# Performance work log

Measured on AMD Instinct MI355X. Metric: run time of the kernel, lower is better.

The kernel has to match this reference:

```python
import jax, jax.numpy as jnp
import numpy as np

DT = 0.001  # forward-arg default in the original module
EPS = 1e-10


def setup_inputs() -> dict:
    key = jax.random.key(0)
    k1, k2 = jax.random.split(key)
    x = jax.random.normal(k1, (5000, 512, 16), dtype=jnp.float32)  # [nt, traces, channels]
    y = jax.random.normal(k2, (5000, 512, 16), dtype=jnp.float32)
    return {"x": x, "y": y}


def reference(x, y):
    # Per-(t,c) L2 norms over time axis (dim 0): shape [T, C]
    xnorm = jnp.linalg.norm(x, ord=2, axis=0) + EPS
    ynorm = jnp.linalg.norm(y, ord=2, axis=0) + EPS
    # Per-(t,c) dot products over time: shape [T, C]
    dots = jnp.einsum('ntc,ntc->tc', x, y)
    # cc = -dot(xn * dt, yn) = -dt * dot(x, y) / (||x|| * ||y||)
    cc = -DT * dots / (xnorm * ynorm)
    # Original skips slices where max|x| == 0 (contributes 0.0)
    mask = jnp.max(jnp.abs(x), axis=0) > 0
    return jnp.sum(jnp.where(mask, cc, jnp.zeros_like(cc)))
```

## Files before the change

kernel.cpp:

```cpp
#include <hip/hip_runtime.h>
#include <hip/hip_bf16.h>
#include <math.h>


#define NT_TOTAL 5000
#define NCOL     8192
#define NCOL4    2048

__global__ __launch_bounds__(256) void ncc_partial(const float4* __restrict__ x,
                                                   const float4* __restrict__ y,
                                                   float4* __restrict__ ws,
                                                   int clen, int nchunk) {
    const int col4 = blockIdx.x * 256 + threadIdx.x;
    const int ch   = blockIdx.y;
    int n0 = ch * clen;
    int n1 = n0 + clen;
    if (n1 > NT_TOTAL) n1 = NT_TOTAL;
    const int steps = (n1 > n0) ? (n1 - n0) : 0;

    const float4* xp = x + (size_t)n0 * NCOL4 + col4;
    const float4* yp = y + (size_t)n0 * NCOL4 + col4;

    float4 sxx = make_float4(0.f, 0.f, 0.f, 0.f);
    float4 syy = make_float4(0.f, 0.f, 0.f, 0.f);
    float4 sxy = make_float4(0.f, 0.f, 0.f, 0.f);
    float4 mx  = make_float4(0.f, 0.f, 0.f, 0.f);

#define ACC(a, b)                                                     \
    sxx.x = fmaf(a.x, a.x, sxx.x); sxx.y = fmaf(a.y, a.y, sxx.y);     \
    sxx.z = fmaf(a.z, a.z, sxx.z); sxx.w = fmaf(a.w, a.w, sxx.w);     \
    syy.x = fmaf(b.x, b.x, syy.x); syy.y = fmaf(b.y, b.y, syy.y);     \
    syy.z = fmaf(b.z, b.z, syy.z); syy.w = fmaf(b.w, b.w, syy.w);     \
    sxy.x = fmaf(a.x, b.x, sxy.x); sxy.y = fmaf(a.y, b.y, sxy.y);     \
    sxy.z = fmaf(a.z, b.z, sxy.z); sxy.w = fmaf(a.w, b.w, sxy.w);     \
    mx.x = fmaxf(mx.x, fabsf(a.x)); mx.y = fmaxf(mx.y, fabsf(a.y));   \
    mx.z = fmaxf(mx.z, fabsf(a.z)); mx.w = fmaxf(mx.w, fabsf(a.w))

    int i = 0;
    for (; i + 8 <= steps; i += 8) {
        float4 a0 = xp[0 * NCOL4];
        float4 a1 = xp[1 * NCOL4];
        float4 a2 = xp[2 * NCOL4];
        float4 a3 = xp[3 * NCOL4];
        float4 a4 = xp[4 * NCOL4];
        float4 a5 = xp[5 * NCOL4];
        float4 a6 = xp[6 * NCOL4];
        float4 a7 = xp[7 * NCOL4];
        float4 b0 = yp[0 * NCOL4];
        float4 b1 = yp[1 * NCOL4];
        float4 b2 = yp[2 * NCOL4];
        float4 b3 = yp[3 * NCOL4];
        float4 b4 = yp[4 * NCOL4];
        float4 b5 = yp[5 * NCOL4];
        float4 b6 = yp[6 * NCOL4];
        float4 b7 = yp[7 * NCOL4];
        xp += 8 * NCOL4;
        yp += 8 * NCOL4;
        ACC(a0, b0); ACC(a1, b1); ACC(a2, b2); ACC(a3, b3);
        ACC(a4, b4); ACC(a5, b5); ACC(a6, b6); ACC(a7, b7);
    }
    for (; i < steps; ++i) {
        float4 a = xp[0];
        float4 b = yp[0];
        xp += NCOL4;
        yp += NCOL4;
        ACC(a, b);
    }
#undef ACC

    float4* SXX = ws;
    float4* SYY = ws + (size_t)nchunk * NCOL4;
    float4* SXY = ws + (size_t)2 * nchunk * NCOL4;
    float4* MX  = ws + (size_t)3 * nchunk * NCOL4;
    const size_t idx = (size_t)ch * NCOL4 + col4;
    SXX[idx] = sxx;
    SYY[idx] = syy;
    SXY[idx] = sxy;
    MX[idx]  = mx;
}

__global__ __launch_bounds__(256) void ncc_combine(const float4* __restrict__ ws4,
                                                   float* __restrict__ partials,
                                                   int nchunk) {
    const int lane  = threadIdx.x & 63;
    const int strip = threadIdx.x >> 6;
    const int c4    = blockIdx.x * 64 + lane;
    const int NC4   = NCOL4;

    const float4* SXX = ws4;
    const float4* SYY = ws4 + (size_t)nchunk * NC4;
    const float4* SXY = ws4 + (size_t)2 * nchunk * NC4;
    const float4* MX  = ws4 + (size_t)3 * nchunk * NC4;

    const int spc = (nchunk + 3) / 4;
    int ch0 = strip * spc;
    int ch1 = ch0 + spc;
    if (ch1 > nchunk) ch1 = nchunk;

    float4 sxx = make_float4(0.f, 0.f, 0.f, 0.f);
    float4 syy = make_float4(0.f, 0.f, 0.f, 0.f);
    float4 sxy = make_float4(0.f, 0.f, 0.f, 0.f);
    float4 mx  = make_float4(0.f, 0.f, 0.f, 0.f);
    for (int ch = ch0; ch < ch1; ++ch) {
        const size_t idx = (size_t)ch * NC4 + c4;
        float4 a = SXX[idx], b = SYY[idx], d = SXY[idx], m = MX[idx];
        sxx.x += a.x; sxx.y += a.y; sxx.z += a.z; sxx.w += a.w;
        syy.x += b.x; syy.y += b.y; syy.z += b.z; syy.w += b.w;
        sxy.x += d.x; sxy.y += d.y; sxy.z += d.z; sxy.w += d.w;
        mx.x = fmaxf(mx.x, m.x); mx.y = fmaxf(mx.y, m.y);
        mx.z = fmaxf(mx.z, m.z); mx.w = fmaxf(mx.w, m.w);
    }

    __shared__ float4 LXX[4][64], LYY[4][64], LXY[4][64], LMX[4][64];
    LXX[strip][lane] = sxx;
    LYY[strip][lane] = syy;
    LXY[strip][lane] = sxy;
    LMX[strip][lane] = mx;
    __syncthreads();

    if (strip == 0) {
        for (int s = 1; s < 4; ++s) {
            float4 a = LXX[s][lane], b = LYY[s][lane], d = LXY[s][lane], m = LMX[s][lane];
            sxx.x += a.x; sxx.y += a.y; sxx.z += a.z; sxx.w += a.w;
            syy.x += b.x; syy.y += b.y; syy.z += b.z; syy.w += b.w;
            sxy.x += d.x; sxy.y += d.y; sxy.z += d.z; sxy.w += d.w;
            mx.x = fmaxf(mx.x, m.x); mx.y = fmaxf(mx.y, m.y);
            mx.z = fmaxf(mx.z, m.z); mx.w = fmaxf(mx.w, m.w);
        }
        float cc = 0.f;
        if (mx.x > 0.f) cc += -0.001f * sxy.x / ((sqrtf(sxx.x) + 1e-10f) * (sqrtf(syy.x) + 1e-10f));
        if (mx.y > 0.f) cc += -0.001f * sxy.y / ((sqrtf(sxx.y) + 1e-10f) * (sqrtf(syy.y) + 1e-10f));
        if (mx.z > 0.f) cc += -0.001f * sxy.z / ((sqrtf(sxx.z) + 1e-10f) * (sqrtf(syy.z) + 1e-10f));
        if (mx.w > 0.f) cc += -0.001f * sxy.w / ((sqrtf(sxx.w) + 1e-10f) * (sqrtf(syy.w) + 1e-10f));

        for (int off = 32; off > 0; off >>= 1)
            cc += __shfl_down(cc, off);
        if (lane == 0)
            partials[blockIdx.x] = cc;
    }
}

__global__ __launch_bounds__(64) void ncc_final(const float* __restrict__ partials,
                                                float* __restrict__ out) {
    float v = (threadIdx.x < 32) ? partials[threadIdx.x] : 0.f;
    for (int off = 32; off > 0; off >>= 1)
        v += __shfl_down(v, off);
    if (threadIdx.x == 0) out[0] = v;
}

extern "C" void kernel_launch(void* const* d_in, const int* in_sizes, int n_in,
                              void* d_out, int out_size, void* d_ws, size_t ws_size,
                              hipStream_t stream) {
    const float* x = (const float*)d_in[0];
    const float* y = (const float*)d_in[1];
    float* out = (float*)d_out;
    float* ws  = (float*)d_ws;

    const size_t per_chunk_bytes = 4ull * NCOL * sizeof(float);
    size_t avail = (ws_size > 256) ? (ws_size - 256) : 0;
    int nchunk = (int)(avail / per_chunk_bytes);
    if (nchunk > 100) nchunk = 100;
    if (nchunk < 1)   nchunk = 1;
    const int clen = (NT_TOTAL + nchunk - 1) / nchunk;

    float* partials = ws + 4ull * (size_t)nchunk * NCOL;

    dim3 g1(NCOL4 / 256, nchunk);
    ncc_partial<<<g1, 256, 0, stream>>>((const float4*)x, (const float4*)y,
                                        (float4*)ws, clen, nchunk);
    ncc_combine<<<32, 256, 0, stream>>>((const float4*)ws, partials, nchunk);
    ncc_final<<<1, 64, 0, stream>>>(partials, out);
}
```

Baseline: 78.22 us.

## Stream inputs via async global-to-LDS loads with double buffering

Replaces direct float4 register loads in the partial-reduction kernel with global_load_lds transfers into double-buffered shared memory. Explicit vmcnt waits overlap the next tile's loads with accumulation of the current one. It also caps the time-chunk count at 64 instead of 100, which reduces the grid size. The cost is more complex synchronisation and fewer resident blocks, which could lower the memory parallelism that hides latency.

```diff
diff --git a/kernel.cpp b/kernel.cpp
--- a/kernel.cpp
+++ b/kernel.cpp
@@ -3,76 +3,108 @@
 #include <math.h>
 
 
-#define NT_TOTAL 5000
+#define NT       5000
+#define NROW_F   8192
 #define NCOL     8192
 #define NCOL4    2048
 
-__global__ __launch_bounds__(256) void ncc_partial(const float4* __restrict__ x,
-                                                   const float4* __restrict__ y,
+typedef __attribute__((address_space(3))) void lds_void;
+typedef const __attribute__((address_space(1))) void gm_void;
+
+__global__ __launch_bounds__(256) void ncc_partial(const float* __restrict__ xg,
+                                                   const float* __restrict__ yg,
                                                    float4* __restrict__ ws,
-                                                   int clen, int nchunk) {
-    const int col4 = blockIdx.x * 256 + threadIdx.x;
+                                                   int clen, int nchunk, int T) {
+    __shared__ float4 BA[4][4][2][64];
+    __shared__ float4 BB[4][4][2][64];
+
+    const int tid  = threadIdx.x;
+    const int w    = tid >> 6;
+    const int lane = tid & 63;
+    const int bx   = blockIdx.x;
     const int ch   = blockIdx.y;
-    int n0 = ch * clen;
-    int n1 = n0 + clen;
-    if (n1 > NT_TOTAL) n1 = NT_TOTAL;
-    const int steps = (n1 > n0) ? (n1 - n0) : 0;
-
-    const float4* xp = x + (size_t)n0 * NCOL4 + col4;
-    const float4* yp = y + (size_t)n0 * NCOL4 + col4;
+    const int n0   = ch * clen;
+    int n1 = n0 + clen; if (n1 > NT) n1 = NT;
+
+    const int colf = bx * 1024 + tid * 4;
 
     float4 sxx = make_float4(0.f, 0.f, 0.f, 0.f);
     float4 syy = make_float4(0.f, 0.f, 0.f, 0.f);
     float4 sxy = make_float4(0.f, 0.f, 0.f, 0.f);
     float4 mx  = make_float4(0.f, 0.f, 0.f, 0.f);
 
-#define ACC(a, b)                                                     \
-    sxx.x = fmaf(a.x, a.x, sxx.x); sxx.y = fmaf(a.y, a.y, sxx.y);     \
-    sxx.z = fmaf(a.z, a.z, sxx.z); sxx.w = fmaf(a.w, a.w, sxx.w);     \
-    syy.x = fmaf(b.x, b.x, syy.x); syy.y = fmaf(b.y, b.y, syy.y);     \
-    syy.z = fmaf(b.z, b.z, syy.z); syy.w = fmaf(b.w, b.w, syy.w);     \
-    sxy.x = fmaf(a.x, b.x, sxy.x); sxy.y = fmaf(a.y, b.y, sxy.y);     \
-    sxy.z = fmaf(a.z, b.z, sxy.z); sxy.w = fmaf(a.w, b.w, sxy.w);     \
-    mx.x = fmaxf(mx.x, fabsf(a.x)); mx.y = fmaxf(mx.y, fabsf(a.y));   \
+#define ACC4(a, b)                                                      \
+    sxx.x = fmaf(a.x, a.x, sxx.x); sxx.y = fmaf(a.y, a.y, sxx.y);       \
+    sxx.z = fmaf(a.z, a.z, sxx.z); sxx.w = fmaf(a.w, a.w, sxx.w);       \
+    syy.x = fmaf(b.x, b.x, syy.x); syy.y = fmaf(b.y, b.y, syy.y);       \
+    syy.z = fmaf(b.z, b.z, syy.z); syy.w = fmaf(b.w, b.w, syy.w);       \
+    sxy.x = fmaf(a.x, b.x, sxy.x); sxy.y = fmaf(a.y, b.y, sxy.y);       \
+    sxy.z = fmaf(a.z, b.z, sxy.z); sxy.w = fmaf(a.w, b.w, sxy.w);       \
+    mx.x = fmaxf(mx.x, fabsf(a.x)); mx.y = fmaxf(mx.y, fabsf(a.y));     \
     mx.z = fmaxf(mx.z, fabsf(a.z)); mx.w = fmaxf(mx.w, fabsf(a.w))
 
-    int i = 0;
-    for (; i + 8 <= steps; i += 8) {
-        float4 a0 = xp[0 * NCOL4];
-        float4 a1 = xp[1 * NCOL4];
-        float4 a2 = xp[2 * NCOL4];
-        float4 a3 = xp[3 * NCOL4];
-        float4 a4 = xp[4 * NCOL4];
-        float4 a5 = xp[5 * NCOL4];
-        float4 a6 = xp[6 * NCOL4];
-        float4 a7 = xp[7 * NCOL4];
-        float4 b0 = yp[0 * NCOL4];
-        float4 b1 = yp[1 * NCOL4];
-        float4 b2 = yp[2 * NCOL4];
-        float4 b3 = yp[3 * NCOL4];
-        float4 b4 = yp[4 * NCOL4];
-        float4 b5 = yp[5 * NCOL4];
-        float4 b6 = yp[6 * NCOL4];
-        float4 b7 = yp[7 * NCOL4];
-        xp += 8 * NCOL4;
-        yp += 8 * NCOL4;
-        ACC(a0, b0); ACC(a1, b1); ACC(a2, b2); ACC(a3, b3);
-        ACC(a4, b4); ACC(a5, b5); ACC(a6, b6); ACC(a7, b7);
-    }
-    for (; i < steps; ++i) {
-        float4 a = xp[0];
-        float4 b = yp[0];
-        xp += NCOL4;
-        yp += NCOL4;
-        ACC(a, b);
-    }
-#undef ACC
+#define ISSUE(BUF, t)                                                         \
+    {                                                                         \
+        _Pragma("unroll")                                                     \
+        for (int r = 0; r < 4; ++r) {                                         \
+            int n = n0 + (t) * 4 + r;                                         \
+            if (n > NT - 1) n = NT - 1;                                       \
+            const float* px = xg + (size_t)n * NROW_F + colf;                 \
+            const float* py = yg + (size_t)n * NROW_F + colf;                 \
+            __builtin_amdgcn_global_load_lds((gm_void*)px,                    \
+                (lds_void*)&BUF[w][r][0][0], 16, 0, 0);                       \
+            __builtin_amdgcn_global_load_lds((gm_void*)py,                    \
+                (lds_void*)&BUF[w][r][1][0], 16, 0, 0);                       \
+        }                                                                     \
+    }
+
+#define COMPUTE(BUF, t)                                                       \
+    {                                                                         \
+        _Pragma("unroll")                                                     \
+        for (int r = 0; r < 4; ++r) {                                         \
+            float4 a = BUF[w][r][0][lane];                                    \
+            float4 b = BUF[w][r][1][lane];                                    \
+            int n = n0 + (t) * 4 + r;                                         \
+            if (n < n1) { ACC4(a, b); }                                       \
+        }                                                                     \
+    }
+
+#define WAITV(N)                                                              \
+    asm volatile("s_waitcnt vmcnt(" #N ")" ::: "memory");                     \
+    __builtin_amdgcn_sched_barrier(0)
+
+#define WAITL()                                                               \
+    asm volatile("s_waitcnt lgkmcnt(0)" ::: "memory");                        \
+    __builtin_amdgcn_sched_barrier(0)
+
+    ISSUE(BA, 0);
+    ISSUE(BB, 1);
+    for (int t = 0; t + 4 <= T; t += 2) {
+        WAITV(8);
+        COMPUTE(BA, t);
+        WAITL();
+        ISSUE(BA, t + 2);
+        WAITV(8);
+        COMPUTE(BB, t + 1);
+        WAITL();
+        ISSUE(BB, t + 3);
+    }
+    WAITV(8);
+    COMPUTE(BA, T - 2);
+    WAITV(0);
+    COMPUTE(BB, T - 1);
+
+#undef ACC4
+#undef ISSUE
+#undef COMPUTE
+#undef WAITV
+#undef WAITL
 
     float4* SXX = ws;
     float4* SYY = ws + (size_t)nchunk * NCOL4;
     float4* SXY = ws + (size_t)2 * nchunk * NCOL4;
     float4* MX  = ws + (size_t)3 * nchunk * NCOL4;
-    const size_t idx = (size_t)ch * NCOL4 + col4;
+    const size_t idx = (size_t)ch * NCOL4 + bx * 256 + tid;
     SXX[idx] = sxx;
     SYY[idx] = syy;
     SXY[idx] = sxy;
@@ -85,12 +117,11 @@
     const int lane  = threadIdx.x & 63;
     const int strip = threadIdx.x >> 6;
     const int c4    = blockIdx.x * 64 + lane;
-    const int NC4   = NCOL4;
 
     const float4* SXX = ws4;
-    const float4* SYY = ws4 + (size_t)nchunk * NC4;
-    const float4* SXY = ws4 + (size_t)2 * nchunk * NC4;
-    const float4* MX  = ws4 + (size_t)3 * nchunk * NC4;
+    const float4* SYY = ws4 + (size_t)nchunk * NCOL4;
+    const float4* SXY = ws4 + (size_t)2 * nchunk * NCOL4;
+    const float4* MX  = ws4 + (size_t)3 * nchunk * NCOL4;
 
     const int spc = (nchunk + 3) / 4;
     int ch0 = strip * spc;
@@ -102,7 +133,7 @@
     float4 sxy = make_float4(0.f, 0.f, 0.f, 0.f);
     float4 mx  = make_float4(0.f, 0.f, 0.f, 0.f);
     for (int ch = ch0; ch < ch1; ++ch) {
-        const size_t idx = (size_t)ch * NC4 + c4;
+        const size_t idx = (size_t)ch * NCOL4 + c4;
         float4 a = SXX[idx], b = SYY[idx], d = SXY[idx], m = MX[idx];
         sxx.x += a.x; sxx.y += a.y; sxx.z += a.z; sxx.w += a.w;
         syy.x += b.x; syy.y += b.y; syy.z += b.z; syy.w += b.w;
@@ -159,15 +190,18 @@
     const size_t per_chunk_bytes = 4ull * NCOL * sizeof(float);
     size_t avail = (ws_size > 256) ? (ws_size - 256) : 0;
     int nchunk = (int)(avail / per_chunk_bytes);
-    if (nchunk > 100) nchunk = 100;
-    if (nchunk < 1)   nchunk = 1;
-    const int clen = (NT_TOTAL + nchunk - 1) / nchunk;
+    if (nchunk > 64) nchunk = 64;
+    if (nchunk < 1)  nchunk = 1;
+    const int clen = (NT + nchunk - 1) / nchunk;
+
+    int T = (clen + 3) / 4;
+    if (T & 1) T++;
+    if (T < 2) T = 2;
 
     float* partials = ws + 4ull * (size_t)nchunk * NCOL;
 
-    dim3 g1(NCOL4 / 256, nchunk);
-    ncc_partial<<<g1, 256, 0, stream>>>((const float4*)x, (const float4*)y,
-                                        (float4*)ws, clen, nchunk);
+    dim3 g1(8, nchunk);
+    ncc_partial<<<g1, 256, 0, stream>>>(x, y, (float4*)ws, clen, nchunk, T);
     ncc_combine<<<32, 256, 0, stream>>>((const float4*)ws, partials, nchunk);
     ncc_final<<<1, 64, 0, stream>>>(partials, out);
 }
```

Measured after the change: 67.38 us. 13.9% less time.
